# Kernel tuning notes

Hardware: AMD Instinct MI355X
Metric: run time of the kernel (lower is better)

The kernel has to match this reference:

```python
import jax, jax.numpy as jnp
import numpy as np

N = 50000    # nodes
E = 800000   # edges per relation
R = 3        # relations
IN, HID, OUT = 128, 128, 64


def setup_inputs() -> dict:
    key = jax.random.key(0)
    ks = jax.random.split(key, 7)
    x = jax.random.normal(ks[0], (N, IN), jnp.float32)
    src = jax.random.randint(ks[1], (R, E), 0, N)
    dst = jax.random.randint(ks[2], (R, E), 0, N)
    W1 = jax.random.normal(ks[3], (R, IN, HID), jnp.float32) / np.sqrt(IN)
    b1 = jnp.zeros((R, HID), jnp.float32)
    W2 = jax.random.normal(ks[4], (R, HID, OUT), jnp.float32) / np.sqrt(HID)
    b2 = jnp.zeros((R, OUT), jnp.float32)
    return {"x": x, "src": src, "dst": dst, "W1": W1, "b1": b1, "W2": W2, "b2": b2}


def _rel_conv(x, src, dst, W, b):
    """dgl GraphConv with norm='both' and self-loops added (dgl.add_self_loop).
    out = D_dst^{-1/2} A_sl (D_src^{-1/2} X W) + b  (weight order commutes)."""
    loop = jnp.arange(N, dtype=src.dtype)
    s = jnp.concatenate([src, loop])  # [E+N] self-loops appended
    d = jnp.concatenate([dst, loop])
    ones = jnp.ones(s.shape[0], x.dtype)
    deg_out = jax.ops.segment_sum(ones, s, num_segments=N)  # >= 1 due to self loops
    deg_in = jax.ops.segment_sum(ones, d, num_segments=N)
    h = (x * jax.lax.rsqrt(deg_out)[:, None]) @ W          # [N, F_out]
    agg = jax.ops.segment_sum(h[s], d, num_segments=N)     # gather-scatter SpMM
    return agg * jax.lax.rsqrt(deg_in)[:, None] + b


def _hetero_layer(x, src, dst, W, b):
    # HeteroGraphConv with aggregate='sum': sum per-relation GraphConv outputs.
    out = _rel_conv(x, src[0], dst[0], W[0], b[0])
    for r in range(1, R):  # small fixed relation count
        out = out + _rel_conv(x, src[r], dst[r], W[r], b[r])
    return out


def reference(x, src, dst, W1, b1, W2, b2):
    h = jax.nn.relu(_hetero_layer(x, src, dst, W1, b1))
    return _hetero_layer(h, src, dst, W2, b2)
```

## Files before the change

### kernel.cpp

```cpp
#include <hip/hip_runtime.h>
#include <hip/hip_fp16.h>


constexpr int N   = 50000;
constexpr int R   = 3;
constexpr int IN  = 128;
constexpr int HID = 128;
constexpr int OUT = 64;
constexpr int M   = R * N;
constexpr int BK  = 1024;
constexpr int NBKT = (M + BK - 1) / BK;
constexpr int CHUNK = 8192;
constexpr int KB  = 24;
constexpr int CVT_N4 = N * IN / 4;
constexpr int WPK   = 6 * KB * 64;
constexpr int WPK_B = (WPK + 255) / 256;

typedef _Float16 half8 __attribute__((ext_vector_type(8)));
typedef float floatx16 __attribute__((ext_vector_type(16)));

__global__ void prep_kernel(const float* __restrict__ x,
                            const float* __restrict__ W1, const float* __restrict__ W2,
                            const float* __restrict__ b1, const float* __restrict__ b2,
                            uint2* __restrict__ x16,
                            __half* __restrict__ F1, __half* __restrict__ F2,
                            float* __restrict__ bsum1, float* __restrict__ bsum2) {
    int b = blockIdx.x;
    if (b == 0) {
        int t = threadIdx.x;
        if (t < HID) bsum1[t] = b1[t] + b1[HID + t] + b1[2 * HID + t];
        if (t < OUT) bsum2[t] = b2[t] + b2[OUT + t] + b2[2 * OUT + t];
        return;
    }
    if (b <= WPK_B) {
        int idx = (b - 1) * 256 + threadIdx.x;
        if (idx < 4 * KB * 64) {
            int nt = idx / (KB * 64), rem = idx % (KB * 64);
            int kb = rem / 64, lane = rem % 64;
            int c = nt * 32 + (lane & 31);
            int k0 = kb * 16 + (lane >> 5) * 8;
            __half h[8];
#pragma unroll
            for (int j = 0; j < 8; j++) h[j] = __float2half_rn(W1[(k0 + j) * 128 + c]);
            *(uint4*)(F1 + (size_t)idx * 8) = *(uint4*)h;
        } else if (idx < 6 * KB * 64) {
            int i2 = idx - 4 * KB * 64;
            int nt = i2 / (KB * 64), rem = i2 % (KB * 64);
            int kb = rem / 64, lane = rem % 64;
            int c = nt * 32 + (lane & 31);
            int k0 = kb * 16 + (lane >> 5) * 8;
            __half h[8];
#pragma unroll
            for (int j = 0; j < 8; j++) h[j] = __float2half_rn(W2[(k0 + j) * 64 + c]);
            *(uint4*)(F2 + (size_t)i2 * 8) = *(uint4*)h;
        }
        return;
    }
    int i = (b - 1 - WPK_B) * 256 + threadIdx.x;
    if (i >= CVT_N4) return;
    float4 v = ((const float4*)x)[i];
    __half2 a = __floats2half2_rn(v.x, v.y);
    __half2 c = __floats2half2_rn(v.z, v.w);
    uint2 o;
    o.x = *(unsigned*)&a;
    o.y = *(unsigned*)&c;
    x16[i] = o;
}

__global__ __launch_bounds__(256) void p1_kernel(const int* __restrict__ src,
                                                 const int* __restrict__ dst,
                                                 int E, int RE, int nb,
                                                 int* __restrict__ bh) {
    __shared__ int hd[NBKT], hs[NBKT];
    for (int i = threadIdx.x; i < NBKT; i += 256) { hd[i] = 0; hs[i] = 0; }
    __syncthreads();
    int beg = blockIdx.x * CHUNK, end = min(RE, beg + CHUNK);
    for (int g = beg + (int)threadIdx.x; g < end; g += 256) {
        int rb = ((g >= E) + (g >= 2 * E)) * N;
        atomicAdd(&hd[(rb + dst[g]) >> 10], 1);
        atomicAdd(&hs[(rb + src[g]) >> 10], 1);
    }
    __syncthreads();
    for (int i = threadIdx.x; i < NBKT; i += 256) {
        bh[i * nb + blockIdx.x] = hd[i];
        bh[(NBKT + i) * nb + blockIdx.x] = hs[i];
    }
}

__global__ void scan1_kernel(const int* __restrict__ in, int* __restrict__ out,
                             int* __restrict__ partials, int L) {
    __shared__ int lds[1024];
    int t = threadIdx.x;
    int idx = blockIdx.x * 1024 + t;
    int v = (idx < L) ? in[idx] : 0;
    lds[t] = v;
    __syncthreads();
    for (int off = 1; off < 1024; off <<= 1) {
        int u = (t >= off) ? lds[t - off] : 0;
        __syncthreads();
        lds[t] += u;
        __syncthreads();
    }
    if (idx < L) out[idx] = lds[t] - v;
    if (t == 1023) partials[blockIdx.x] = lds[1023];
}

__global__ void scan2_kernel(int* __restrict__ partials, int nb1) {
    __shared__ int lds[256];
    int t = threadIdx.x;
    int v = (t < nb1) ? partials[t] : 0;
    lds[t] = v;
    __syncthreads();
    for (int off = 1; off < 256; off <<= 1) {
        int u = (t >= off) ? lds[t - off] : 0;
        __syncthreads();
        lds[t] += u;
        __syncthreads();
    }
    if (t < nb1) partials[t] = lds[t] - v;
}

__global__ __launch_bounds__(256) void p3_kernel(const int* __restrict__ src,
                                                 const int* __restrict__ dst,
                                                 int E, int RE, int nb,
                                                 const int* __restrict__ scanv,
                                                 const int* __restrict__ partials,
                                                 int* __restrict__ ebd,
                                                 unsigned short* __restrict__ ebs) {
    __shared__ int cd[NBKT], cs[NBKT];
    for (int i = threadIdx.x; i < NBKT; i += 256) {
        int id = i * nb + blockIdx.x;
        int is = (NBKT + i) * nb + blockIdx.x;
        cd[i] = scanv[id] + partials[id >> 10];
        cs[i] = scanv[is] + partials[is >> 10] - RE;
    }
    __syncthreads();
    int beg = blockIdx.x * CHUNK, end = min(RE, beg + CHUNK);
    for (int g = beg + (int)threadIdx.x; g < end; g += 256) {
        int rb = ((g >= E) + (g >= 2 * E)) * N;
        int s  = src[g];
        int kd = rb + dst[g];
        int pd = atomicAdd(&cd[kd >> 10], 1);
        ebd[pd] = (s << 10) | (kd & 1023);
        int ks = rb + s;
        int ps = atomicAdd(&cs[ks >> 10], 1);
        ebs[ps] = (unsigned short)(ks & 1023);
    }
}

__global__ __launch_bounds__(1024) void pbs_kernel(const int* __restrict__ scanv,
                                                   const int* __restrict__ partials,
                                                   int nb, int RE,
                                                   const unsigned short* __restrict__ ebs,
                                                   float* __restrict__ rs_out) {
    __shared__ int cnt[BK];
    int t = threadIdx.x;
    int k = blockIdx.x;
    int i0 = (NBKT + k) * nb;
    int segbeg = scanv[i0] + partials[i0 >> 10] - RE;
    int segend;
    if (k == NBKT - 1) segend = RE;
    else {
        int i1 = i0 + nb;
        segend = scanv[i1] + partials[i1 >> 10] - RE;
    }
    cnt[t] = 0;
    __syncthreads();
    for (int e = segbeg + t; e < segend; e += 1024)
        atomicAdd(&cnt[(int)ebs[e]], 1);
    __syncthreads();
    int slot = k * BK + t;
    if (slot < M) rs_out[slot] = rsqrtf((float)(cnt[t] + 1));
}

__global__ __launch_bounds__(1024) void pbd_kernel(const int* __restrict__ scanv,
                                                   const int* __restrict__ partials,
                                                   int nb, int RE,
                                                   const int* __restrict__ ebd,
                                                   const float* __restrict__ rs_out,
                                                   int* __restrict__ row_ptr,
                                                   float* __restrict__ rs_in,
                                                   unsigned int* __restrict__ esrc) {
    __shared__ int cnt[BK];
    __shared__ int cur[BK];
    int t = threadIdx.x;
    int k = blockIdx.x;
    int i0 = k * nb;
    int segbeg = scanv[i0] + partials[i0 >> 10];
    int segend;
    if (k == NBKT - 1) segend = RE;
    else {
        int i1 = (k + 1) * nb;
        segend = scanv[i1] + partials[i1 >> 10];
    }
    cnt[t] = 0;
    __syncthreads();
    for (int e = segbeg + t; e < segend; e += 1024)
        atomicAdd(&cnt[ebd[e] & 1023], 1);
    __syncthreads();
    int slot = k * BK + t;
    int c = cnt[t];
    cur[t] = c;
    __syncthreads();
    for (int off = 1; off < 1024; off <<= 1) {
        int u = (t >= off) ? cur[t - off] : 0;
        __syncthreads();
        cur[t] += u;
        __syncthreads();
    }
    int excl = cur[t] - c;
    if (slot < M) {
        row_ptr[slot] = segbeg + excl;
        rs_in[slot] = rsqrtf((float)(c + 1));
    }
    if (k == NBKT - 1 && t == 0) row_ptr[M] = RE;
    __syncthreads();
    cur[t] = segbeg + excl;
    __syncthreads();
    for (int e = segbeg + t; e < segend; e += 1024) {
        int v = ebd[e];
        int key = k * BK + (v & 1023);
        int r = (key >= 2 * N) + (key >= N);
        unsigned s = (unsigned)(v >> 10);
        int pos = atomicAdd(&cur[v & 1023], 1);
        __half h = __float2half_rn(rs_out[r * N + s]);
        esrc[pos] = s | ((unsigned)__half_as_ushort(h) << 16);
    }
}

__global__ __launch_bounds__(256) void gather_kernel(const __half* __restrict__ Xh,
                                                     const float* __restrict__ rs_in,
                                                     const float* __restrict__ rs_out,
                                                     const int* __restrict__ row_ptr,
                                                     const unsigned int* __restrict__ esrc,
                                                     __half* __restrict__ Z16) {
    int n = blockIdx.x * 4 + (threadIdx.x >> 6);
    if (n >= N) return;
    int lane = threadIdx.x & 63;
    int pair = lane >> 5;
    int c4 = (lane & 31) * 4;
    uint2 xn = *(const uint2*)(Xh + (long)n * 128 + c4);
    const __half2 z2 = __float2half2_rn(0.f);
#pragma unroll
    for (int r = 0; r < R; r++) {
        int key = r * N + n;
        __half2 acc0 = z2, acc1 = z2;
        int beg = row_ptr[key], end = row_ptr[key + 1];
        int e = beg;
        for (; e + 16 <= end; e += 16) {
            unsigned u[8];
            uint2 y[8];
#pragma unroll
            for (int j = 0; j < 8; j++) u[j] = esrc[e + 2 * j + pair];
#pragma unroll
            for (int j = 0; j < 8; j++)
                y[j] = *(const uint2*)(Xh + (long)(u[j] & 0xffffu) * 128 + c4);
#pragma unroll
            for (int j = 0; j < 8; j++) {
                __half2 cj = __half2half2(__ushort_as_half((unsigned short)(u[j] >> 16)));
                acc0 = __hfma2(*(__half2*)&y[j].x, cj, acc0);
                acc1 = __hfma2(*(__half2*)&y[j].y, cj, acc1);
            }
        }
        for (; e + 8 <= end; e += 8) {
            unsigned u[4];
            uint2 y[4];
#pragma unroll
            for (int j = 0; j < 4; j++) u[j] = esrc[e + 2 * j + pair];
#pragma unroll
            for (int j = 0; j < 4; j++)
                y[j] = *(const uint2*)(Xh + (long)(u[j] & 0xffffu) * 128 + c4);
#pragma unroll
            for (int j = 0; j < 4; j++) {
                __half2 cj = __half2half2(__ushort_as_half((unsigned short)(u[j] >> 16)));
                acc0 = __hfma2(*(__half2*)&y[j].x, cj, acc0);
                acc1 = __hfma2(*(__half2*)&y[j].y, cj, acc1);
            }
        }
        for (; e < end; e += 2) {
            int idx = e + pair;
            unsigned u = (idx < end) ? esrc[idx] : 0u;
            uint2 y = *(const uint2*)(Xh + (long)(u & 0xffffu) * 128 + c4);
            __half2 cc = __half2half2(__ushort_as_half((unsigned short)(u >> 16)));
            acc0 = __hfma2(*(__half2*)&y.x, cc, acc0);
            acc1 = __hfma2(*(__half2*)&y.y, cc, acc1);
        }
        unsigned a0 = *(unsigned*)&acc0, a1 = *(unsigned*)&acc1;
        unsigned b0 = (unsigned)__shfl_xor((int)a0, 32, 64);
        unsigned b1 = (unsigned)__shfl_xor((int)a1, 32, 64);
        acc0 = __hadd2(acc0, *(__half2*)&b0);
        acc1 = __hadd2(acc1, *(__half2*)&b1);
        __half2 cs = __float2half2_rn(rs_out[key]);
        acc0 = __hfma2(*(__half2*)&xn.x, cs, acc0);
        acc1 = __hfma2(*(__half2*)&xn.y, cs, acc1);
        __half2 ri = __float2half2_rn(rs_in[key]);
        acc0 = __hmul2(acc0, ri);
        acc1 = __hmul2(acc1, ri);
        if (pair == 0) {
            uint2 o;
            o.x = *(unsigned*)&acc0;
            o.y = *(unsigned*)&acc1;
            *(uint2*)(Z16 + (long)n * 384 + r * 128 + c4) = o;
        }
    }
}

__global__ __launch_bounds__(256) void mfma_gemm1_kernel(const __half* __restrict__ Z16,
                                                         const __half* __restrict__ F,
                                                         const float* __restrict__ bias,
                                                         __half* __restrict__ H16) {
    int wave = threadIdx.x >> 6, lane = threadIdx.x & 63;
    int m0 = blockIdx.x * 128 + wave * 32;
    int mr = min(m0 + (lane & 31), N - 1);
    const half8* A = (const half8*)(Z16 + (long)mr * 384 + (lane >> 5) * 8);
    const half8* B = (const half8*)F;
    floatx16 acc[4];
#pragma unroll
    for (int i = 0; i < 4; i++)
#pragma unroll
        for (int j = 0; j < 16; j++) acc[i][j] = 0.f;

    half8 a = A[0];
    for (int kb = 0; kb < KB; kb++) {
        half8 an = (kb < KB - 1) ? A[(kb + 1) * 2] : a;
#pragma unroll
        for (int nt = 0; nt < 4; nt++) {
            half8 b = B[(nt * KB + kb) * 64 + lane];
            acc[nt] = __builtin_amdgcn_mfma_f32_32x32x16_f16(a, b, acc[nt], 0, 0, 0);
        }
        a = an;
    }
    float bv[4];
#pragma unroll
    for (int nt = 0; nt < 4; nt++) bv[nt] = bias[nt * 32 + (lane & 31)];
    int rbase = m0 + 4 * (lane >> 5);
    int col0 = lane & 31;
#pragma unroll
    for (int nt = 0; nt < 4; nt++) {
#pragma unroll
        for (int reg = 0; reg < 16; reg++) {
            int row = rbase + (reg & 3) + 8 * (reg >> 2);
            if (row < N) {
                float v = fmaxf(acc[nt][reg] + bv[nt], 0.f);
                H16[(long)row * 128 + nt * 32 + col0] = __float2half_rn(v);
            }
        }
    }
}

__global__ __launch_bounds__(256) void mfma_gemmY_kernel(const __half* __restrict__ H16,
                                                         const __half* __restrict__ F,
                                                         __half* __restrict__ Y2) {
    int wave = threadIdx.x >> 6, lane = threadIdx.x & 63;
    int r = blockIdx.y;
    int m0 = blockIdx.x * 128 + wave * 32;
    int mr = min(m0 + (lane & 31), N - 1);
    const half8* A = (const half8*)(H16 + (long)mr * 128 + (lane >> 5) * 8);
    const half8* B = (const half8*)F;
    floatx16 acc[2];
#pragma unroll
    for (int i = 0; i < 2; i++)
#pragma unroll
        for (int j = 0; j < 16; j++) acc[i][j] = 0.f;

#pragma unroll
    for (int kbr = 0; kbr < 8; kbr++) {
        half8 a = A[kbr * 2];
#pragma unroll
        for (int nt = 0; nt < 2; nt++) {
            half8 b = B[(nt * KB + r * 8 + kbr) * 64 + lane];
            acc[nt] = __builtin_amdgcn_mfma_f32_32x32x16_f16(a, b, acc[nt], 0, 0, 0);
        }
    }
    int rbase = m0 + 4 * (lane >> 5);
    int col0 = lane & 31;
    __half* Yr = Y2 + (long)r * N * 64;
#pragma unroll
    for (int nt = 0; nt < 2; nt++) {
#pragma unroll
        for (int reg = 0; reg < 16; reg++) {
            int row = rbase + (reg & 3) + 8 * (reg >> 2);
            if (row < N)
                Yr[(long)row * 64 + nt * 32 + col0] = __float2half_rn(acc[nt][reg]);
        }
    }
}

__global__ __launch_bounds__(256) void gather_out_kernel(const __half* __restrict__ Y2,
                                                         const float* __restrict__ rs_in,
                                                         const float* __restrict__ rs_out,
                                                         const int* __restrict__ row_ptr,
                                                         const unsigned int* __restrict__ esrc,
                                                         const float* __restrict__ bias,
                                                         float* __restrict__ outp) {
    int n = blockIdx.x * 4 + (threadIdx.x >> 6);
    if (n >= N) return;
    int lane = threadIdx.x & 63;
    int pair = lane >> 5;
    int c2 = (lane & 31) * 2;
    const __half2 z2 = __float2half2_rn(0.f);
    float2 tot = ((const float2*)bias)[lane & 31];
#pragma unroll
    for (int r = 0; r < R; r++) {
        int key = r * N + n;
        const __half* Yr = Y2 + (long)r * N * 64;
        __half2 acc = z2;
        int beg = row_ptr[key], end = row_ptr[key + 1];
        int e = beg;
        for (; e + 16 <= end; e += 16) {
            unsigned u[8];
            __half2 y[8];
#pragma unroll
            for (int j = 0; j < 8; j++) u[j] = esrc[e + 2 * j + pair];
#pragma unroll
            for (int j = 0; j < 8; j++)
                y[j] = *(const __half2*)(Yr + (long)(u[j] & 0xffffu) * 64 + c2);
#pragma unroll
            for (int j = 0; j < 8; j++)
                acc = __hfma2(y[j], __half2half2(__ushort_as_half((unsigned short)(u[j] >> 16))), acc);
        }
        for (; e + 8 <= end; e += 8) {
            unsigned u[4];
            __half2 y[4];
#pragma unroll
            for (int j = 0; j < 4; j++) u[j] = esrc[e + 2 * j + pair];
#pragma unroll
            for (int j = 0; j < 4; j++)
                y[j] = *(const __half2*)(Yr + (long)(u[j] & 0xffffu) * 64 + c2);
#pragma unroll
            for (int j = 0; j < 4; j++)
                acc = __hfma2(y[j], __half2half2(__ushort_as_half((unsigned short)(u[j] >> 16))), acc);
        }
        for (; e < end; e += 2) {
            int idx = e + pair;
            unsigned u = (idx < end) ? esrc[idx] : 0u;
            __half2 y = *(const __half2*)(Yr + (long)(u & 0xffffu) * 64 + c2);
            acc = __hfma2(y, __half2half2(__ushort_as_half((unsigned short)(u >> 16))), acc);
        }
        unsigned a0 = *(unsigned*)&acc;
        unsigned b0 = (unsigned)__shfl_xor((int)a0, 32, 64);
        acc = __hadd2(acc, *(__half2*)&b0);
        __half2 ys = *(const __half2*)(Yr + (long)n * 64 + c2);
        acc = __hfma2(ys, __float2half2_rn(rs_out[key]), acc);
        float2 f = __half22float2(acc);
        float ri = rs_in[key];
        tot.x += ri * f.x;
        tot.y += ri * f.y;
    }
    if (pair == 0) *(float2*)(outp + (long)n * 64 + c2) = tot;
}

extern "C" void kernel_launch(void* const* d_in, const int* in_sizes, int n_in,
                              void* d_out, int out_size, void* d_ws, size_t ws_size,
                              hipStream_t stream) {
    const float* x  = (const float*)d_in[0];
    const int*  src = (const int*)d_in[1];
    const int*  dst = (const int*)d_in[2];
    const float* W1 = (const float*)d_in[3];
    const float* b1 = (const float*)d_in[4];
    const float* W2 = (const float*)d_in[5];
    const float* b2 = (const float*)d_in[6];
    float* out = (float*)d_out;
    const int E  = in_sizes[1] / R;
    const int RE = in_sizes[1];
    const int nb = (RE + CHUNK - 1) / CHUNK;
    const int L  = 2 * NBKT * nb;
    const int nb1 = (L + 1023) / 1024;

    char* ws = (char*)d_ws;
    size_t off = 0;
    auto alloc = [&](size_t bytes) -> void* {
        void* p = ws + off;
        off += (bytes + 255) & ~(size_t)255;
        return p;
    };
    float* bsum1    = (float*)alloc(HID * 4);
    float* bsum2    = (float*)alloc(OUT * 4);
    float* rs_in    = (float*)alloc((size_t)M * 4);
    float* rs_out   = (float*)alloc((size_t)M * 4);
    int*   row_ptr  = (int*)alloc((size_t)(M + 1) * 4);
    int*   bh       = (int*)alloc((size_t)L * 4);
    int*   scanv    = (int*)alloc((size_t)L * 4);
    int*   partials = (int*)alloc((size_t)nb1 * 4);
    unsigned* esrc  = (unsigned*)alloc((size_t)RE * 4);
    __half* F1      = (__half*)alloc((size_t)4 * KB * 64 * 8 * 2);
    __half* F2      = (__half*)alloc((size_t)2 * KB * 64 * 8 * 2);
    char*  regA     = (char*)alloc((size_t)N * 384 * 2);
    int*   ebd      = (int*)regA;
    unsigned short* ebs = (unsigned short*)(regA + (size_t)RE * 4);
    __half* Z16     = (__half*)regA;
    __half* Y2      = (__half*)regA;
    __half* x16     = (__half*)alloc((size_t)N * IN * 2);
    __half* H16     = (__half*)alloc((size_t)N * HID * 2);

    prep_kernel<<<1 + WPK_B + (CVT_N4 + 255) / 256, 256, 0, stream>>>(
        x, W1, W2, b1, b2, (uint2*)x16, F1, F2, bsum1, bsum2);
    p1_kernel<<<nb, 256, 0, stream>>>(src, dst, E, RE, nb, bh);
    scan1_kernel<<<nb1, 1024, 0, stream>>>(bh, scanv, partials, L);
    scan2_kernel<<<1, 256, 0, stream>>>(partials, nb1);
    p3_kernel<<<nb, 256, 0, stream>>>(src, dst, E, RE, nb, scanv, partials, ebd, ebs);
    pbs_kernel<<<NBKT, 1024, 0, stream>>>(scanv, partials, nb, RE, ebs, rs_out);
    pbd_kernel<<<NBKT, 1024, 0, stream>>>(scanv, partials, nb, RE, ebd, rs_out,
                                          row_ptr, rs_in, esrc);

    const int ab  = (N + 3) / 4;
    const int ggb = (N + 127) / 128;

    gather_kernel<<<ab, 256, 0, stream>>>(x16, rs_in, rs_out, row_ptr, esrc, Z16);
    mfma_gemm1_kernel<<<ggb, 256, 0, stream>>>(Z16, F1, bsum1, H16);
    mfma_gemmY_kernel<<<dim3(ggb, R), 256, 0, stream>>>(H16, F2, Y2);
    gather_out_kernel<<<ab, 256, 0, stream>>>(Y2, rs_in, rs_out, row_ptr, esrc,
                                              bsum2, out);
}
```

Before: 372.1 us.

## Split layer-1 gather into four feature-quarter passes for cache locality

The fp16 input features are stored as four column quarters of 32 features each, every quarter a separate contiguous [N,32] array. The layer-1 gather kernel now runs four passes over the grid's y dimension, each handling one quarter, so the gathered working set per pass is smaller and more likely to stay in L2/MALL. Each wave now processes 8 edges at a time with 8 lanes per edge, replacing 2 edges with 32 lanes, and reduces across lane groups with three shuffles. The cost is re-reading the edge lists and row pointers four times and issuing smaller 64-byte row fetches.

```diff
diff --git a/kernel.cpp b/kernel.cpp
--- a/kernel.cpp
+++ b/kernel.cpp
@@ -15,6 +15,8 @@
 constexpr int CVT_N4 = N * IN / 4;
 constexpr int WPK   = 6 * KB * 64;
 constexpr int WPK_B = (WPK + 255) / 256;
+constexpr int NPASS = 4;
+constexpr int QC    = IN / NPASS;
 
 typedef _Float16 half8 __attribute__((ext_vector_type(8)));
 typedef float floatx16 __attribute__((ext_vector_type(16)));
@@ -22,7 +24,7 @@
 __global__ void prep_kernel(const float* __restrict__ x,
                             const float* __restrict__ W1, const float* __restrict__ W2,
                             const float* __restrict__ b1, const float* __restrict__ b2,
-                            uint2* __restrict__ x16,
+                            __half* __restrict__ x16,
                             __half* __restrict__ F1, __half* __restrict__ F2,
                             float* __restrict__ bsum1, float* __restrict__ bsum2) {
     int b = blockIdx.x;
@@ -64,7 +66,11 @@
     uint2 o;
     o.x = *(unsigned*)&a;
     o.y = *(unsigned*)&c;
-    x16[i] = o;
+    int n  = i >> 5;
+    int c4 = (i & 31) * 4;
+    int q  = c4 >> 5;
+    int cq = c4 & 31;
+    *(uint2*)(x16 + (size_t)q * N * QC + (size_t)n * QC + cq) = o;
 }
 
 __global__ __launch_bounds__(256) void p1_kernel(const int* __restrict__ src,
@@ -236,10 +242,12 @@
                                                      __half* __restrict__ Z16) {
     int n = blockIdx.x * 4 + (threadIdx.x >> 6);
     if (n >= N) return;
+    int q = blockIdx.y;
     int lane = threadIdx.x & 63;
-    int pair = lane >> 5;
-    int c4 = (lane & 31) * 4;
-    uint2 xn = *(const uint2*)(Xh + (long)n * 128 + c4);
+    int g = lane >> 3;
+    int cl = lane & 7;
+    const __half* Xq = Xh + (size_t)q * N * QC;
+    uint2 xn = *(const uint2*)(Xq + (long)n * QC + cl * 4);
     const __half2 z2 = __float2half2_rn(0.f);
 #pragma unroll
     for (int r = 0; r < R; r++) {
@@ -248,59 +256,44 @@
         int beg = row_ptr[key], end = row_ptr[key + 1];
         int e = beg;
         for (; e + 16 <= end; e += 16) {
-            unsigned u[8];
-            uint2 y[8];
-#pragma unroll
-            for (int j = 0; j < 8; j++) u[j] = esrc[e + 2 * j + pair];
-#pragma unroll
-            for (int j = 0; j < 8; j++)
-                y[j] = *(const uint2*)(Xh + (long)(u[j] & 0xffffu) * 128 + c4);
-#pragma unroll
-            for (int j = 0; j < 8; j++) {
-                __half2 cj = __half2half2(__ushort_as_half((unsigned short)(u[j] >> 16)));
-                acc0 = __hfma2(*(__half2*)&y[j].x, cj, acc0);
-                acc1 = __hfma2(*(__half2*)&y[j].y, cj, acc1);
-            }
-        }
-        for (; e + 8 <= end; e += 8) {
-            unsigned u[4];
-            uint2 y[4];
-#pragma unroll
-            for (int j = 0; j < 4; j++) u[j] = esrc[e + 2 * j + pair];
-#pragma unroll
-            for (int j = 0; j < 4; j++)
-                y[j] = *(const uint2*)(Xh + (long)(u[j] & 0xffffu) * 128 + c4);
-#pragma unroll
-            for (int j = 0; j < 4; j++) {
-                __half2 cj = __half2half2(__ushort_as_half((unsigned short)(u[j] >> 16)));
-                acc0 = __hfma2(*(__half2*)&y[j].x, cj, acc0);
-                acc1 = __hfma2(*(__half2*)&y[j].y, cj, acc1);
-            }
-        }
-        for (; e < end; e += 2) {
-            int idx = e + pair;
+            unsigned u0 = esrc[e + g];
+            unsigned u1 = esrc[e + 8 + g];
+            uint2 y0 = *(const uint2*)(Xq + (long)(u0 & 0xffffu) * QC + cl * 4);
+            uint2 y1 = *(const uint2*)(Xq + (long)(u1 & 0xffffu) * QC + cl * 4);
+            __half2 c0 = __half2half2(__ushort_as_half((unsigned short)(u0 >> 16)));
+            __half2 c1 = __half2half2(__ushort_as_half((unsigned short)(u1 >> 16)));
+            acc0 = __hfma2(*(__half2*)&y0.x, c0, acc0);
+            acc1 = __hfma2(*(__half2*)&y0.y, c0, acc1);
+            acc0 = __hfma2(*(__half2*)&y1.x, c1, acc0);
+            acc1 = __hfma2(*(__half2*)&y1.y, c1, acc1);
+        }
+        for (; e < end; e += 8) {
+            int idx = e + g;
             unsigned u = (idx < end) ? esrc[idx] : 0u;
-            uint2 y = *(const uint2*)(Xh + (long)(u & 0xffffu) * 128 + c4);
+            uint2 y = *(const uint2*)(Xq + (long)(u & 0xffffu) * QC + cl * 4);
             __half2 cc = __half2half2(__ushort_as_half((unsigned short)(u >> 16)));
             acc0 = __hfma2(*(__half2*)&y.x, cc, acc0);
             acc1 = __hfma2(*(__half2*)&y.y, cc, acc1);
         }
-        unsigned a0 = *(unsigned*)&acc0, a1 = *(unsigned*)&acc1;
-        unsigned b0 = (unsigned)__shfl_xor((int)a0, 32, 64);
-        unsigned b1 = (unsigned)__shfl_xor((int)a1, 32, 64);
-        acc0 = __hadd2(acc0, *(__half2*)&b0);
-        acc1 = __hadd2(acc1, *(__half2*)&b1);
+#pragma unroll
+        for (int off = 8; off < 64; off <<= 1) {
+            unsigned a0 = *(unsigned*)&acc0, a1 = *(unsigned*)&acc1;
+            unsigned b0 = (unsigned)__shfl_xor((int)a0, off, 64);
+            unsigned b1 = (unsigned)__shfl_xor((int)a1, off, 64);
+            acc0 = __hadd2(acc0, *(__half2*)&b0);
+            acc1 = __hadd2(acc1, *(__half2*)&b1);
+        }
         __half2 cs = __float2half2_rn(rs_out[key]);
         acc0 = __hfma2(*(__half2*)&xn.x, cs, acc0);
         acc1 = __hfma2(*(__half2*)&xn.y, cs, acc1);
         __half2 ri = __float2half2_rn(rs_in[key]);
         acc0 = __hmul2(acc0, ri);
         acc1 = __hmul2(acc1, ri);
-        if (pair == 0) {
+        if (g == 0) {
             uint2 o;
             o.x = *(unsigned*)&acc0;
             o.y = *(unsigned*)&acc1;
-            *(uint2*)(Z16 + (long)n * 384 + r * 128 + c4) = o;
+            *(uint2*)(Z16 + (long)n * 384 + r * 128 + q * QC + cl * 4) = o;
         }
     }
 }
@@ -494,7 +487,7 @@
     __half* H16     = (__half*)alloc((size_t)N * HID * 2);
 
     prep_kernel<<<1 + WPK_B + (CVT_N4 + 255) / 256, 256, 0, stream>>>(
-        x, W1, W2, b1, b2, (uint2*)x16, F1, F2, bsum1, bsum2);
+        x, W1, W2, b1, b2, x16, F1, F2, bsum1, bsum2);
     p1_kernel<<<nb, 256, 0, stream>>>(src, dst, E, RE, nb, bh);
     scan1_kernel<<<nb1, 1024, 0, stream>>>(bh, scanv, partials, L);
     scan2_kernel<<<1, 256, 0, stream>>>(partials, nb1);
@@ -506,7 +499,8 @@
     const int ab  = (N + 3) / 4;
     const int ggb = (N + 127) / 128;
 
-    gather_kernel<<<ab, 256, 0, stream>>>(x16, rs_in, rs_out, row_ptr, esrc, Z16);
+    gather_kernel<<<dim3(ab, NPASS), 256, 0, stream>>>(x16, rs_in, rs_out, row_ptr,
+                                                       esrc, Z16);
     mfma_gemm1_kernel<<<ggb, 256, 0, stream>>>(Z16, F1, bsum1, H16);
     mfma_gemmY_kernel<<<dim3(ggb, R), 256, 0, stream>>>(H16, F2, Y2);
     gather_out_kernel<<<ab, 256, 0, stream>>>(Y2, rs_in, rs_out, row_ptr, esrc,
```

Result: slower. 456.7 us (+22.8%).
